# Kernel optimization log

Hardware: AMD Instinct MI355X
Metric: run time of the kernel (lower is better)

The kernel has to match this reference:

```python
import jax, jax.numpy as jnp
import numpy as np

C = 512
NUM_HEADS = 8


def setup_inputs() -> dict:
    key = jax.random.key(0)
    ks = jax.random.split(key, 9)
    s = 1.0 / np.sqrt(C)
    inp = {
        "x": jax.random.normal(ks[0], (2, C, 64, 64), dtype=jnp.float32),
        "Wq": jax.random.uniform(ks[1], (C, C), jnp.float32, -s, s),
        "bq": jax.random.uniform(ks[2], (C,), jnp.float32, -s, s),
        "Wk": jax.random.uniform(ks[3], (C, C), jnp.float32, -s, s),
        "bk": jax.random.uniform(ks[4], (C,), jnp.float32, -s, s),
        "Wv": jax.random.uniform(ks[5], (C, C), jnp.float32, -s, s),
        "bv": jax.random.uniform(ks[6], (C,), jnp.float32, -s, s),
        "Wp": jax.random.uniform(ks[7], (C, C), jnp.float32, -s, s),
        "bp": jax.random.uniform(ks[8], (C,), jnp.float32, -s, s),
    }
    return inp


def _split_heads(t):
    # [B, S, C] -> [B, h, S, d]
    B, S, Ct = t.shape
    return t.reshape(B, S, NUM_HEADS, Ct // NUM_HEADS).transpose(0, 2, 1, 3)


def reference(x, Wq, bq, Wk, bk, Wv, bv, Wp, bp):
    B, Ct, H, W = x.shape
    tok = x.transpose(0, 2, 3, 1).reshape(B, H * W, Ct)  # [B, S, C]
    q = _split_heads(tok @ Wq.T + bq)
    k = _split_heads(tok @ Wk.T + bk)
    v = _split_heads(tok @ Wv.T + bv)
    d = q.shape[-1]
    scores = jnp.einsum("bhsd,bhtd->bhst", q, k) / jnp.sqrt(jnp.float32(d))
    attn = jax.nn.softmax(scores, axis=-1)
    out = jnp.einsum("bhst,bhtd->bhsd", attn, v)
    out = out.transpose(0, 2, 1, 3).reshape(B, H * W, Ct)  # merge heads
    out = out @ Wp.T + bp
    return out.reshape(B, H, W, Ct).transpose(0, 3, 1, 2)
```

## Files before the change

### kernel.cpp

```cpp
#include <hip/hip_runtime.h>
#include <stdint.h>
#include <math.h>

typedef unsigned short u16;
typedef uint32_t u32;
typedef short bf16x8 __attribute__((ext_vector_type(8)));
typedef float f32x4  __attribute__((ext_vector_type(4)));

#define DEV __device__ __forceinline__

DEV u16 f2bf(float f) {
    union { float f; u32 u; } x; x.f = f;
    u32 lsb = (x.u >> 16) & 1u;
    x.u += 0x7fffu + lsb;
    return (u16)(x.u >> 16);
}

DEV u32 pack2(float a, float b) {
    union { float f; u32 u; } x, y; x.f = a; y.f = b;
    return __builtin_amdgcn_perm(y.u + 0x8000u, x.u + 0x8000u, 0x07060302u);
}

#if __has_builtin(__builtin_amdgcn_exp2f)
DEV float fexp2(float x) { return __builtin_amdgcn_exp2f(x); }
#else
DEV float fexp2(float x) { return __expf(x * 0.69314718056f); }
#endif

DEV f32x4 mfma16(bf16x8 a, bf16x8 b, f32x4 c) {
    return __builtin_amdgcn_mfma_f32_16x16x32_bf16(a, b, c, 0, 0, 0);
}

__global__ __launch_bounds__(256) void prep_kernel(const float* __restrict__ x,
                                                   u16* __restrict__ tok,
                                                   const float* __restrict__ w0,
                                                   const float* __restrict__ w1,
                                                   const float* __restrict__ w2,
                                                   const float* __restrict__ w3,
                                                   u16* __restrict__ dst) {
    __shared__ u16 t[64][65];
    const int id = blockIdx.x, tid = threadIdx.x;
    if (id < 1024) {
        const int b = id >> 9, c0 = ((id >> 6) & 7) * 64, s0 = (id & 63) * 64;
        const float* xb = x + ((size_t)b * 512 + c0) * 4096 + s0;
        u16* tb = tok + ((size_t)b * 4096 + s0) * 512 + c0;
        {
            const int jc = tid & 15, i0 = tid >> 4;
#pragma unroll
            for (int ii = 0; ii < 4; ii++) {
                int i = i0 * 4 + ii;
                float4 v = *(const float4*)&xb[(size_t)i * 4096 + jc * 4];
                t[i][jc * 4 + 0] = f2bf(v.x);
                t[i][jc * 4 + 1] = f2bf(v.y);
                t[i][jc * 4 + 2] = f2bf(v.z);
                t[i][jc * 4 + 3] = f2bf(v.w);
            }
        }
        __syncthreads();
        {
            const int j = tid & 31, i0 = tid >> 5;
#pragma unroll
            for (int ii = 0; ii < 8; ii++) {
                int srow = i0 * 8 + ii;
                u32 v = (u32)t[j * 2][srow] | ((u32)t[j * 2 + 1][srow] << 16);
                *(u32*)(&tb[(size_t)srow * 512 + j * 2]) = v;
            }
        }
    } else {
        const int id2 = id - 1024;
        const int j = id2 >> 8;
        const float* src = (j == 0) ? w0 : (j == 1) ? w1 : (j == 2) ? w2 : w3;
        int idx = ((id2 & 255) * 256 + tid) * 4;
        float4 v = *(const float4*)&src[idx];
        uint2 pv;
        pv.x = pack2(v.x, v.y);
        pv.y = pack2(v.z, v.w);
        *(uint2*)&dst[(size_t)j * 262144 + idx] = pv;
    }
}

DEV void proj_core(const u16* __restrict__ W, const float* __restrict__ bias,
                   const u16* __restrict__ Bb, void* __restrict__ out,
                   int b, int mode, float scale,
                   u16 (*__restrict__ Alds)[4096], u16 (*__restrict__ Blds)[4096]) {
    const int tid = threadIdx.x;
    const int wave = tid >> 6, lane = tid & 63, q = lane >> 4, c = lane & 15;
    const int m0 = blockIdx.y * 128, n0 = blockIdx.x * 128;

    const int cs = tid & 15, qs = (tid >> 4) & 3, ms = (tid >> 6) & 3;
    const u16* Asrc0 = W  + (size_t)(m0 + ms * 16 + cs) * 512 + qs * 8;
    const u16* Asrc1 = W  + (size_t)(m0 + (ms + 4) * 16 + cs) * 512 + qs * 8;
    const u16* Bsrc0 = Bb + (size_t)(n0 + ms * 16 + cs) * 512 + qs * 8;
    const u16* Bsrc1 = Bb + (size_t)(n0 + (ms + 4) * 16 + cs) * 512 + qs * 8;

    f32x4 acc[4][4] = {};

    int4 pa0 = *(const int4*)&Asrc0[0];
    int4 pa1 = *(const int4*)&Asrc1[0];
    int4 pb0 = *(const int4*)&Bsrc0[0];
    int4 pb1 = *(const int4*)&Bsrc1[0];
    int4 ha0 = *(const int4*)&Asrc0[32];
    int4 ha1 = *(const int4*)&Asrc1[32];
    int4 hb0 = *(const int4*)&Bsrc0[32];
    int4 hb1 = *(const int4*)&Bsrc1[32];
    *(int4*)&Alds[0][tid * 8]         = pa0;
    *(int4*)&Alds[0][(tid + 256) * 8] = pa1;
    *(int4*)&Blds[0][tid * 8]         = pb0;
    *(int4*)&Blds[0][(tid + 256) * 8] = pb1;
    __syncthreads();

    int p = 0, pw = 1;
    for (int it = 0; it < 16; it++) {
        const int kn = ((it + 2) & 15) * 32;

        int4 na0 = *(const int4*)&Asrc0[kn];
        int4 na1 = *(const int4*)&Asrc1[kn];
        int4 nb0 = *(const int4*)&Bsrc0[kn];
        int4 nb1 = *(const int4*)&Bsrc1[kn];

        bf16x8 af[4], bfr[4];
#pragma unroll
        for (int t = 0; t < 4; t++) {
            int gm = (((wave & 1) * 4 + t) * 4 + q) * 16 + c;
            af[t] = *(const bf16x8*)&Alds[p][gm * 8];
            int gn = (((wave >> 1) * 4 + t) * 4 + q) * 16 + c;
            bfr[t] = *(const bf16x8*)&Blds[p][gn * 8];
        }
#pragma unroll
        for (int mt = 0; mt < 4; mt++)
#pragma unroll
            for (int nt = 0; nt < 4; nt++)
                acc[mt][nt] = mfma16(af[mt], bfr[nt], acc[mt][nt]);

        *(int4*)&Alds[pw][tid * 8]         = ha0;
        *(int4*)&Alds[pw][(tid + 256) * 8] = ha1;
        *(int4*)&Blds[pw][tid * 8]         = hb0;
        *(int4*)&Blds[pw][(tid + 256) * 8] = hb1;
        ha0 = na0; ha1 = na1; hb0 = nb0; hb1 = nb1;
        __syncthreads();
        p = pw; pw = (pw == 2) ? 0 : pw + 1;
    }

    const int mbase = m0 + (wave & 1) * 64, nbase = n0 + (wave >> 1) * 64;
#pragma unroll
    for (int mt = 0; mt < 4; mt++) {
        int co0 = mbase + mt * 16 + q * 4;
        float b0 = bias[co0 + 0], b1 = bias[co0 + 1];
        float b2 = bias[co0 + 2], b3 = bias[co0 + 3];
#pragma unroll
        for (int nt = 0; nt < 4; nt++) {
            int scol = nbase + nt * 16 + c;
            float v0 = (acc[mt][nt][0] + b0) * scale;
            float v1 = (acc[mt][nt][1] + b1) * scale;
            float v2 = (acc[mt][nt][2] + b2) * scale;
            float v3 = (acc[mt][nt][3] + b3) * scale;
            if (mode == 0) {
                uint2 pv; pv.x = pack2(v0, v1); pv.y = pack2(v2, v3);
                size_t idx = ((size_t)(b * 8 + (co0 >> 6)) * 4096 + scol) * 64 + (co0 & 63);
                *(uint2*)&((u16*)out)[idx] = pv;
            } else if (mode == 1) {
                u16* o = (u16*)out;
                o[((size_t)(b * 512 + co0 + 0)) * 4096 + scol] = f2bf(v0);
                o[((size_t)(b * 512 + co0 + 1)) * 4096 + scol] = f2bf(v1);
                o[((size_t)(b * 512 + co0 + 2)) * 4096 + scol] = f2bf(v2);
                o[((size_t)(b * 512 + co0 + 3)) * 4096 + scol] = f2bf(v3);
            } else {
                float* o = (float*)out;
                o[((size_t)(b * 512 + co0 + 0)) * 4096 + scol] = v0;
                o[((size_t)(b * 512 + co0 + 1)) * 4096 + scol] = v1;
                o[((size_t)(b * 512 + co0 + 2)) * 4096 + scol] = v2;
                o[((size_t)(b * 512 + co0 + 3)) * 4096 + scol] = v3;
            }
        }
    }
}

__global__ __launch_bounds__(256) void qkv_kernel(const u16* __restrict__ Wbf,
                                                  const float* __restrict__ bq,
                                                  const float* __restrict__ bk,
                                                  const float* __restrict__ bv,
                                                  const u16* __restrict__ tok,
                                                  u16* __restrict__ Qb,
                                                  u16* __restrict__ Kb,
                                                  u16* __restrict__ Vb) {
    __shared__ u16 Alds[3][4096];
    __shared__ u16 Blds[3][4096];
    const int z = blockIdx.z, j = z >> 1, b = z & 1;
    const u16* W = Wbf + (size_t)j * 262144;
    const float* bias = (j == 0) ? bq : (j == 1) ? bk : bv;
    void* out = (j == 0) ? (void*)Qb : (j == 1) ? (void*)Kb : (void*)Vb;
    const float scale = (j == 0) ? 0.1803368801f : 1.0f;
    const int mode = (j == 2) ? 1 : 0;
    proj_core(W, bias, tok + (size_t)b * (4096 * 512), out, b, mode, scale, Alds, Blds);
}

__global__ __launch_bounds__(256) void projp_kernel(const u16* __restrict__ Wp,
                                                    const float* __restrict__ bp,
                                                    const u16* __restrict__ attout,
                                                    float* __restrict__ out) {
    __shared__ u16 Alds[3][4096];
    __shared__ u16 Blds[3][4096];
    const int b = blockIdx.z;
    proj_core(Wp, bp, attout + (size_t)b * (4096 * 512), out, b, 2, 1.0f, Alds, Blds);
}

__global__ __launch_bounds__(256, 4) void attn_kernel(const u16* __restrict__ Qm,
                                                      const u16* __restrict__ Km,
                                                      const u16* __restrict__ Vm,
                                                      float* __restrict__ Opart,
                                                      float* __restrict__ Lpart) {
    __shared__ u16 Klds[2][4096];
    __shared__ u16 Vlds[2][4096];
    __shared__ u16 Plds[4][1024];
    const int tid = threadIdx.x, wave = tid >> 6, lane = tid & 63;
    const int q = lane >> 4, c = lane & 15;
    const int bhd = blockIdx.y, s0 = blockIdx.x * 128, z = blockIdx.z;
    const int tbase = z * 2048;
    const u16* Qb = Qm + (size_t)bhd * (4096 * 64);
    const u16* Kb = Km + (size_t)bhd * (4096 * 64);
    const u16* Vb = Vm + (size_t)bhd * (64 * 4096);

    bf16x8 qf[2][2];
#pragma unroll
    for (int st = 0; st < 2; st++)
#pragma unroll
        for (int kd = 0; kd < 2; kd++)
            qf[st][kd] = *(const bf16x8*)
                &Qb[(size_t)(s0 + wave * 32 + st * 16 + c) * 64 + kd * 32 + q * 8];

    const int rr = tid & 15, qq = (tid >> 4) & 3, kk = (tid >> 6) & 1;
    const int t40 = tid >> 7, t41 = t40 + 2;
    const u16* Ksrc0 = Kb + (size_t)(tbase + t40 * 16 + rr) * 64 + kk * 32 + qq * 8;
    const u16* Ksrc1 = Kb + (size_t)(tbase + t41 * 16 + rr) * 64 + kk * 32 + qq * 8;
    const u16* Vsrc0 = Vb + (size_t)(t40 * 16 + rr) * 4096 + tbase + kk * 32 + qq * 8;
    const u16* Vsrc1 = Vb + (size_t)(t41 * 16 + rr) * 4096 + tbase + kk * 32 + qq * 8;

    u16* Pwr       = &Plds[wave][(q >> 1) * 128 + (q & 1) * 4 + c * 8];
    const u16* Prd = &Plds[wave][q * 128 + c * 8];

    f32x4 oacc[4][2] = {};
    float lsum[2] = {0.f, 0.f};

    *(int4*)&Klds[0][tid * 8]         = *(const int4*)&Ksrc0[0];
    *(int4*)&Klds[0][(tid + 256) * 8] = *(const int4*)&Ksrc1[0];
    *(int4*)&Vlds[0][tid * 8]         = *(const int4*)&Vsrc0[0];
    *(int4*)&Vlds[0][(tid + 256) * 8] = *(const int4*)&Vsrc1[0];
    __syncthreads();

    for (int it = 0; it < 32; it++) {
        const int p = it & 1;
        const size_t t0n = (size_t)(((it + 1) & 31) * 64);

        int4 kst0 = *(const int4*)&Ksrc0[t0n * 64];
        int4 kst1 = *(const int4*)&Ksrc1[t0n * 64];
        int4 vst0 = *(const int4*)&Vsrc0[t0n];
        int4 vst1 = *(const int4*)&Vsrc1[t0n];

        f32x4 sacc[4][2] = {};
#pragma unroll
        for (int kd = 0; kd < 2; kd++) {
            bf16x8 ka[4];
#pragma unroll
            for (int tt = 0; tt < 4; tt++)
                ka[tt] = *(const bf16x8*)&Klds[p][(((tt * 2 + kd) * 4 + q) * 16 + c) * 8];
#pragma unroll
            for (int tt = 0; tt < 4; tt++)
#pragma unroll
                for (int st = 0; st < 2; st++)
                    sacc[tt][st] = mfma16(ka[tt], qf[st][kd], sacc[tt][st]);
        }

        bf16x8 va[2][4];
#pragma unroll
        for (int kt = 0; kt < 2; kt++)
#pragma unroll
            for (int dt = 0; dt < 4; dt++)
                va[kt][dt] = *(const bf16x8*)&Vlds[p][(((dt * 2 + kt) * 4 + q) * 16 + c) * 8];

#pragma unroll
        for (int st = 0; st < 2; st++) {
#pragma unroll
            for (int tt = 0; tt < 4; tt++) {
                float p0 = fexp2(sacc[tt][st][0]);
                float p1 = fexp2(sacc[tt][st][1]);
                float p2 = fexp2(sacc[tt][st][2]);
                float p3 = fexp2(sacc[tt][st][3]);
                lsum[st] += (p0 + p1) + (p2 + p3);
                uint2 pv; pv.x = pack2(p0, p1); pv.y = pack2(p2, p3);
                *(uint2*)&Pwr[tt * 256] = pv;
            }
#pragma unroll
            for (int kt = 0; kt < 2; kt++) {
                bf16x8 pb = *(const bf16x8*)&Prd[kt * 512];
#pragma unroll
                for (int dt = 0; dt < 4; dt++)
                    oacc[dt][st] = mfma16(va[kt][dt], pb, oacc[dt][st]);
            }
        }

        *(int4*)&Klds[1 - p][tid * 8]         = kst0;
        *(int4*)&Klds[1 - p][(tid + 256) * 8] = kst1;
        *(int4*)&Vlds[1 - p][tid * 8]         = vst0;
        *(int4*)&Vlds[1 - p][(tid + 256) * 8] = vst1;
        __syncthreads();
    }

#pragma unroll
    for (int st = 0; st < 2; st++) {
        float l = lsum[st];
        l += __shfl_xor(l, 16, 64);
        l += __shfl_xor(l, 32, 64);
        const int s = s0 + wave * 32 + st * 16 + c;
        const size_t rowbase = ((size_t)(z * 16 + bhd) * 4096 + s) * 64;
#pragma unroll
        for (int dt = 0; dt < 4; dt++) {
            float4 ov;
            ov.x = oacc[dt][st][0];
            ov.y = oacc[dt][st][1];
            ov.z = oacc[dt][st][2];
            ov.w = oacc[dt][st][3];
            *(float4*)&Opart[rowbase + dt * 16 + q * 4] = ov;
        }
        if (lane < 16)
            Lpart[(size_t)z * 65536 + bhd * 4096 + s0 + wave * 32 + st * 16 + lane] = l;
    }
}

__global__ __launch_bounds__(256) void merge_kernel(const float* __restrict__ Opart,
                                                    const float* __restrict__ Lpart,
                                                    u16* __restrict__ attout) {
    const int i = blockIdx.x * 256 + threadIdx.x;
    const int flat = i * 4;
    const int row = flat >> 6, dv = flat & 63;
    const int bhd = row >> 12, s = row & 4095;
    const float l = Lpart[row] + Lpart[65536 + row];
    const float rl = 1.0f / l;
    const float4 a  = *(const float4*)&Opart[flat];
    const float4 b4 = *(const float4*)&Opart[4194304 + flat];
    uint2 pv;
    pv.x = pack2((a.x + b4.x) * rl, (a.y + b4.y) * rl);
    pv.y = pack2((a.z + b4.z) * rl, (a.w + b4.w) * rl);
    const int b = bhd >> 3, hd = bhd & 7;
    *(uint2*)&attout[((size_t)(b * 4096 + s)) * 512 + hd * 64 + dv] = pv;
}

extern "C" void kernel_launch(void* const* d_in, const int* in_sizes, int n_in,
                              void* d_out, int out_size, void* d_ws, size_t ws_size,
                              hipStream_t stream) {
    (void)in_sizes; (void)n_in; (void)out_size; (void)ws_size;
    const float* x  = (const float*)d_in[0];
    const float* Wq = (const float*)d_in[1];
    const float* bq = (const float*)d_in[2];
    const float* Wk = (const float*)d_in[3];
    const float* bk = (const float*)d_in[4];
    const float* Wv = (const float*)d_in[5];
    const float* bv = (const float*)d_in[6];
    const float* Wp = (const float*)d_in[7];
    const float* bp = (const float*)d_in[8];
    float* out = (float*)d_out;

    const size_t NTOK = (size_t)4 * 1024 * 1024;
    u16* tok = (u16*)d_ws;
    u16* Qb  = tok + NTOK;
    u16* Kb  = Qb + NTOK;
    u16* Vb  = Kb + NTOK;
    u16* Wbf = Vb + NTOK;
    u16* attout = tok;
    float* Opart = (float*)(Wbf + 4 * 262144);
    float* Lpart = Opart + (size_t)2 * 4194304;

    prep_kernel<<<dim3(2048), 256, 0, stream>>>(x, tok, Wq, Wk, Wv, Wp, Wbf);
    qkv_kernel<<<dim3(32, 4, 6), 256, 0, stream>>>(Wbf, bq, bk, bv, tok, Qb, Kb, Vb);
    attn_kernel<<<dim3(32, 16, 2), 256, 0, stream>>>(Qb, Kb, Vb, Opart, Lpart);
    merge_kernel<<<dim3(4096), 256, 0, stream>>>(Opart, Lpart, attout);
    projp_kernel<<<dim3(32, 4, 2), 256, 0, stream>>>(Wbf + 3 * 262144, bp, attout, out);
}
```

Before: 221.0 us.

## Use direct global-to-LDS loads in GEMM and attention; halve projection N-tile

```diff
diff --git a/kernel.cpp b/kernel.cpp
--- a/kernel.cpp
+++ b/kernel.cpp
@@ -8,6 +8,10 @@
 typedef float f32x4  __attribute__((ext_vector_type(4)));
 
 #define DEV __device__ __forceinline__
+
+#define AS1 __attribute__((address_space(1)))
+#define AS3 __attribute__((address_space(3)))
+#define GLOAD16(g, l) __builtin_amdgcn_global_load_lds((const AS1 void*)(g), (AS3 void*)(l), 16, 0, 0)
 
 DEV u16 f2bf(float f) {
     union { float f; u32 u; } x; x.f = f;
@@ -79,13 +83,16 @@
     }
 }
 
+template<int NFR>
 DEV void proj_core(const u16* __restrict__ W, const float* __restrict__ bias,
                    const u16* __restrict__ Bb, void* __restrict__ out,
                    int b, int mode, float scale,
-                   u16 (*__restrict__ Alds)[4096], u16 (*__restrict__ Blds)[4096]) {
+                   u16* __restrict__ Alds, u16* __restrict__ Blds) {
     const int tid = threadIdx.x;
     const int wave = tid >> 6, lane = tid & 63, q = lane >> 4, c = lane & 15;
-    const int m0 = blockIdx.y * 128, n0 = blockIdx.x * 128;
+    const int m0 = blockIdx.y * 128, n0 = blockIdx.x * (NFR * 32);
+    const int BSTR = NFR * 1024;
+    const int wbase = (tid & ~63) * 8;
 
     const int cs = tid & 15, qs = (tid >> 4) & 3, ms = (tid >> 6) & 3;
     const u16* Asrc0 = W  + (size_t)(m0 + ms * 16 + cs) * 512 + qs * 8;
@@ -93,62 +100,55 @@
     const u16* Bsrc0 = Bb + (size_t)(n0 + ms * 16 + cs) * 512 + qs * 8;
     const u16* Bsrc1 = Bb + (size_t)(n0 + (ms + 4) * 16 + cs) * 512 + qs * 8;
 
-    f32x4 acc[4][4] = {};
-
-    int4 pa0 = *(const int4*)&Asrc0[0];
-    int4 pa1 = *(const int4*)&Asrc1[0];
-    int4 pb0 = *(const int4*)&Bsrc0[0];
-    int4 pb1 = *(const int4*)&Bsrc1[0];
-    int4 ha0 = *(const int4*)&Asrc0[32];
-    int4 ha1 = *(const int4*)&Asrc1[32];
-    int4 hb0 = *(const int4*)&Bsrc0[32];
-    int4 hb1 = *(const int4*)&Bsrc1[32];
-    *(int4*)&Alds[0][tid * 8]         = pa0;
-    *(int4*)&Alds[0][(tid + 256) * 8] = pa1;
-    *(int4*)&Blds[0][tid * 8]         = pb0;
-    *(int4*)&Blds[0][(tid + 256) * 8] = pb1;
+    f32x4 acc[4][NFR] = {};
+
+    GLOAD16(Asrc0, Alds + wbase);
+    GLOAD16(Asrc1, Alds + wbase + 2048);
+    GLOAD16(Bsrc0, Blds + wbase);
+    if (NFR == 4) GLOAD16(Bsrc1, Blds + wbase + 2048);
     __syncthreads();
 
-    int p = 0, pw = 1;
     for (int it = 0; it < 16; it++) {
-        const int kn = ((it + 2) & 15) * 32;
-
-        int4 na0 = *(const int4*)&Asrc0[kn];
-        int4 na1 = *(const int4*)&Asrc1[kn];
-        int4 nb0 = *(const int4*)&Bsrc0[kn];
-        int4 nb1 = *(const int4*)&Bsrc1[kn];
-
-        bf16x8 af[4], bfr[4];
+        const int p = it & 1;
+        const int kn = ((it + 1) & 15) * 32;
+
+        u16* Ad = Alds + (1 - p) * 4096 + wbase;
+        u16* Bd = Blds + (1 - p) * BSTR + wbase;
+        GLOAD16(Asrc0 + kn, Ad);
+        GLOAD16(Asrc1 + kn, Ad + 2048);
+        GLOAD16(Bsrc0 + kn, Bd);
+        if (NFR == 4) GLOAD16(Bsrc1 + kn, Bd + 2048);
+
+        const u16* Ap = Alds + p * 4096;
+        const u16* Bp = Blds + p * BSTR;
+        bf16x8 af[4], bfr[NFR];
 #pragma unroll
         for (int t = 0; t < 4; t++) {
             int gm = (((wave & 1) * 4 + t) * 4 + q) * 16 + c;
-            af[t] = *(const bf16x8*)&Alds[p][gm * 8];
-            int gn = (((wave >> 1) * 4 + t) * 4 + q) * 16 + c;
-            bfr[t] = *(const bf16x8*)&Blds[p][gn * 8];
+            af[t] = *(const bf16x8*)&Ap[gm * 8];
+        }
+#pragma unroll
+        for (int t = 0; t < NFR; t++) {
+            int gn = (((wave >> 1) * NFR + t) * 4 + q) * 16 + c;
+            bfr[t] = *(const bf16x8*)&Bp[gn * 8];
         }
 #pragma unroll
         for (int mt = 0; mt < 4; mt++)
 #pragma unroll
-            for (int nt = 0; nt < 4; nt++)
+            for (int nt = 0; nt < NFR; nt++)
                 acc[mt][nt] = mfma16(af[mt], bfr[nt], acc[mt][nt]);
 
-        *(int4*)&Alds[pw][tid * 8]         = ha0;
-        *(int4*)&Alds[pw][(tid + 256) * 8] = ha1;
-        *(int4*)&Blds[pw][tid * 8]         = hb0;
-        *(int4*)&Blds[pw][(tid + 256) * 8] = hb1;
-        ha0 = na0; ha1 = na1; hb0 = nb0; hb1 = nb1;
         __syncthreads();
-        p = pw; pw = (pw == 2) ? 0 : pw + 1;
-    }
-
-    const int mbase = m0 + (wave & 1) * 64, nbase = n0 + (wave >> 1) * 64;
+    }
+
+    const int mbase = m0 + (wave & 1) * 64, nbase = n0 + (wave >> 1) * (NFR * 16);
 #pragma unroll
     for (int mt = 0; mt < 4; mt++) {
         int co0 = mbase + mt * 16 + q * 4;
         float b0 = bias[co0 + 0], b1 = bias[co0 + 1];
         float b2 = bias[co0 + 2], b3 = bias[co0 + 3];
 #pragma unroll
-        for (int nt = 0; nt < 4; nt++) {
+        for (int nt = 0; nt < NFR; nt++) {
             int scol = nbase + nt * 16 + c;
             float v0 = (acc[mt][nt][0] + b0) * scale;
             float v1 = (acc[mt][nt][1] + b1) * scale;
@@ -183,25 +183,25 @@
                                                   u16* __restrict__ Qb,
                                                   u16* __restrict__ Kb,
                                                   u16* __restrict__ Vb) {
-    __shared__ u16 Alds[3][4096];
-    __shared__ u16 Blds[3][4096];
+    __shared__ u16 Alds[2 * 4096];
+    __shared__ u16 Blds[2 * 4096];
     const int z = blockIdx.z, j = z >> 1, b = z & 1;
     const u16* W = Wbf + (size_t)j * 262144;
     const float* bias = (j == 0) ? bq : (j == 1) ? bk : bv;
     void* out = (j == 0) ? (void*)Qb : (j == 1) ? (void*)Kb : (void*)Vb;
     const float scale = (j == 0) ? 0.1803368801f : 1.0f;
     const int mode = (j == 2) ? 1 : 0;
-    proj_core(W, bias, tok + (size_t)b * (4096 * 512), out, b, mode, scale, Alds, Blds);
+    proj_core<4>(W, bias, tok + (size_t)b * (4096 * 512), out, b, mode, scale, Alds, Blds);
 }
 
 __global__ __launch_bounds__(256) void projp_kernel(const u16* __restrict__ Wp,
                                                     const float* __restrict__ bp,
                                                     const u16* __restrict__ attout,
                                                     float* __restrict__ out) {
-    __shared__ u16 Alds[3][4096];
-    __shared__ u16 Blds[3][4096];
+    __shared__ u16 Alds[2 * 4096];
+    __shared__ u16 Blds[2 * 2048];
     const int b = blockIdx.z;
-    proj_core(Wp, bp, attout + (size_t)b * (4096 * 512), out, b, 2, 1.0f, Alds, Blds);
+    proj_core<2>(Wp, bp, attout + (size_t)b * (4096 * 512), out, b, 2, 1.0f, Alds, Blds);
 }
 
 __global__ __launch_bounds__(256, 4) void attn_kernel(const u16* __restrict__ Qm,
@@ -216,6 +216,7 @@
     const int q = lane >> 4, c = lane & 15;
     const int bhd = blockIdx.y, s0 = blockIdx.x * 128, z = blockIdx.z;
     const int tbase = z * 2048;
+    const int wbase = (tid & ~63) * 8;
     const u16* Qb = Qm + (size_t)bhd * (4096 * 64);
     const u16* Kb = Km + (size_t)bhd * (4096 * 64);
     const u16* Vb = Vm + (size_t)bhd * (64 * 4096);
@@ -241,20 +242,20 @@
     f32x4 oacc[4][2] = {};
     float lsum[2] = {0.f, 0.f};
 
-    *(int4*)&Klds[0][tid * 8]         = *(const int4*)&Ksrc0[0];
-    *(int4*)&Klds[0][(tid + 256) * 8] = *(const int4*)&Ksrc1[0];
-    *(int4*)&Vlds[0][tid * 8]         = *(const int4*)&Vsrc0[0];
-    *(int4*)&Vlds[0][(tid + 256) * 8] = *(const int4*)&Vsrc1[0];
+    GLOAD16(Ksrc0, &Klds[0][wbase]);
+    GLOAD16(Ksrc1, &Klds[0][wbase + 2048]);
+    GLOAD16(Vsrc0, &Vlds[0][wbase]);
+    GLOAD16(Vsrc1, &Vlds[0][wbase + 2048]);
     __syncthreads();
 
     for (int it = 0; it < 32; it++) {
         const int p = it & 1;
         const size_t t0n = (size_t)(((it + 1) & 31) * 64);
 
-        int4 kst0 = *(const int4*)&Ksrc0[t0n * 64];
-        int4 kst1 = *(const int4*)&Ksrc1[t0n * 64];
-        int4 vst0 = *(const int4*)&Vsrc0[t0n];
-        int4 vst1 = *(const int4*)&Vsrc1[t0n];
+        GLOAD16(Ksrc0 + t0n * 64, &Klds[1 - p][wbase]);
+        GLOAD16(Ksrc1 + t0n * 64, &Klds[1 - p][wbase + 2048]);
+        GLOAD16(Vsrc0 + t0n,      &Vlds[1 - p][wbase]);
+        GLOAD16(Vsrc1 + t0n,      &Vlds[1 - p][wbase + 2048]);
 
         f32x4 sacc[4][2] = {};
 #pragma unroll
@@ -298,10 +299,6 @@
             }
         }
 
-        *(int4*)&Klds[1 - p][tid * 8]         = kst0;
-        *(int4*)&Klds[1 - p][(tid + 256) * 8] = kst1;
-        *(int4*)&Vlds[1 - p][tid * 8]         = vst0;
-        *(int4*)&Vlds[1 - p][(tid + 256) * 8] = vst1;
         __syncthreads();
     }
 
@@ -373,5 +370,5 @@
     qkv_kernel<<<dim3(32, 4, 6), 256, 0, stream>>>(Wbf, bq, bk, bv, tok, Qb, Kb, Vb);
     attn_kernel<<<dim3(32, 16, 2), 256, 0, stream>>>(Qb, Kb, Vb, Opart, Lpart);
     merge_kernel<<<dim3(4096), 256, 0, stream>>>(Opart, Lpart, attout);
-    projp_kernel<<<dim3(32, 4, 2), 256, 0, stream>>>(Wbf + 3 * 262144, bp, attout, out);
-}
+    projp_kernel<<<dim3(64, 4, 2), 256, 0, stream>>>(Wbf + 3 * 262144, bp, attout, out);
+}
```

After: 232.3 us. 5.1% more time.

## Fuse Q, K, V projections into one kernel sharing token tiles

Applied to the files above, without the earlier changes.

```diff
diff --git a/kernel.cpp b/kernel.cpp
--- a/kernel.cpp
+++ b/kernel.cpp
@@ -79,6 +79,124 @@
     }
 }
 
+__global__ __launch_bounds__(256, 2) void qkv3_kernel(const u16* __restrict__ Wbf,
+                                                      const float* __restrict__ bq,
+                                                      const float* __restrict__ bk,
+                                                      const float* __restrict__ bv,
+                                                      const u16* __restrict__ tok,
+                                                      u16* __restrict__ Qb,
+                                                      u16* __restrict__ Kb,
+                                                      u16* __restrict__ Vb) {
+    __shared__ u16 Alds[3][6144];
+    __shared__ u16 Blds[3][4096];
+    const int tid = threadIdx.x;
+    const int wave = tid >> 6, lane = tid & 63, q = lane >> 4, c = lane & 15;
+    const int n0 = blockIdx.x * 128;
+    const int m0 = blockIdx.y * 64;
+    const int b  = blockIdx.z;
+    const u16* tokb = tok + (size_t)b * (4096 * 512);
+
+    const int cs = tid & 15, qs = (tid >> 4) & 3, ms = tid >> 6;
+    const u16* As0 = Wbf +          (size_t)(m0 + ms * 16 + cs) * 512 + qs * 8;
+    const u16* As1 = Wbf + 262144 + (size_t)(m0 + ms * 16 + cs) * 512 + qs * 8;
+    const u16* As2 = Wbf + 524288 + (size_t)(m0 + ms * 16 + cs) * 512 + qs * 8;
+    const u16* Bsrc0 = tokb + (size_t)(n0 + ms * 16 + cs) * 512 + qs * 8;
+    const u16* Bsrc1 = tokb + (size_t)(n0 + (ms + 4) * 16 + cs) * 512 + qs * 8;
+
+    f32x4 acc[3][2][4] = {};
+
+    int4 pA0 = *(const int4*)&As0[0];
+    int4 pA1 = *(const int4*)&As1[0];
+    int4 pA2 = *(const int4*)&As2[0];
+    int4 pB0 = *(const int4*)&Bsrc0[0];
+    int4 pB1 = *(const int4*)&Bsrc1[0];
+    int4 hA0 = *(const int4*)&As0[32];
+    int4 hA1 = *(const int4*)&As1[32];
+    int4 hA2 = *(const int4*)&As2[32];
+    int4 hB0 = *(const int4*)&Bsrc0[32];
+    int4 hB1 = *(const int4*)&Bsrc1[32];
+    *(int4*)&Alds[0][tid * 8]        = pA0;
+    *(int4*)&Alds[0][2048 + tid * 8] = pA1;
+    *(int4*)&Alds[0][4096 + tid * 8] = pA2;
+    *(int4*)&Blds[0][tid * 8]         = pB0;
+    *(int4*)&Blds[0][(tid + 256) * 8] = pB1;
+    __syncthreads();
+
+    int p = 0, pw = 1;
+    for (int it = 0; it < 16; it++) {
+        const int kn = ((it + 2) & 15) * 32;
+
+        int4 nA0 = *(const int4*)&As0[kn];
+        int4 nA1 = *(const int4*)&As1[kn];
+        int4 nA2 = *(const int4*)&As2[kn];
+        int4 nB0 = *(const int4*)&Bsrc0[kn];
+        int4 nB1 = *(const int4*)&Bsrc1[kn];
+
+        bf16x8 bfr[4];
+#pragma unroll
+        for (int t = 0; t < 4; t++) {
+            int gn = (((wave >> 1) * 4 + t) * 4 + q) * 16 + c;
+            bfr[t] = *(const bf16x8*)&Blds[p][gn * 8];
+        }
+#pragma unroll
+        for (int j = 0; j < 3; j++) {
+            bf16x8 af[2];
+#pragma unroll
+            for (int mt = 0; mt < 2; mt++) {
+                int gm = ((((wave & 1) * 2 + mt) * 4 + q) * 16 + c);
+                af[mt] = *(const bf16x8*)&Alds[p][j * 2048 + gm * 8];
+            }
+#pragma unroll
+            for (int mt = 0; mt < 2; mt++)
+#pragma unroll
+                for (int nt = 0; nt < 4; nt++)
+                    acc[j][mt][nt] = mfma16(af[mt], bfr[nt], acc[j][mt][nt]);
+        }
+
+        *(int4*)&Alds[pw][tid * 8]        = hA0;
+        *(int4*)&Alds[pw][2048 + tid * 8] = hA1;
+        *(int4*)&Alds[pw][4096 + tid * 8] = hA2;
+        *(int4*)&Blds[pw][tid * 8]         = hB0;
+        *(int4*)&Blds[pw][(tid + 256) * 8] = hB1;
+        hA0 = nA0; hA1 = nA1; hA2 = nA2; hB0 = nB0; hB1 = nB1;
+        __syncthreads();
+        p = pw; pw = (pw == 2) ? 0 : pw + 1;
+    }
+
+    const int mbase = m0 + (wave & 1) * 32, nbase = n0 + (wave >> 1) * 64;
+    const int hd = m0 >> 6;
+#pragma unroll
+    for (int j = 0; j < 3; j++) {
+        const float* bias = (j == 0) ? bq : (j == 1) ? bk : bv;
+        const float scale = (j == 0) ? 0.1803368801f : 1.0f;
+        u16* outm = (j == 0) ? Qb : Kb;
+#pragma unroll
+        for (int mt = 0; mt < 2; mt++) {
+            int co0 = mbase + mt * 16 + q * 4;
+            float b0 = bias[co0 + 0], b1 = bias[co0 + 1];
+            float b2 = bias[co0 + 2], b3 = bias[co0 + 3];
+#pragma unroll
+            for (int nt = 0; nt < 4; nt++) {
+                int scol = nbase + nt * 16 + c;
+                float v0 = (acc[j][mt][nt][0] + b0) * scale;
+                float v1 = (acc[j][mt][nt][1] + b1) * scale;
+                float v2 = (acc[j][mt][nt][2] + b2) * scale;
+                float v3 = (acc[j][mt][nt][3] + b3) * scale;
+                if (j < 2) {
+                    uint2 pv; pv.x = pack2(v0, v1); pv.y = pack2(v2, v3);
+                    size_t idx = ((size_t)(b * 8 + hd) * 4096 + scol) * 64 + (co0 & 63);
+                    *(uint2*)&outm[idx] = pv;
+                } else {
+                    Vb[((size_t)(b * 512 + co0 + 0)) * 4096 + scol] = f2bf(v0);
+                    Vb[((size_t)(b * 512 + co0 + 1)) * 4096 + scol] = f2bf(v1);
+                    Vb[((size_t)(b * 512 + co0 + 2)) * 4096 + scol] = f2bf(v2);
+                    Vb[((size_t)(b * 512 + co0 + 3)) * 4096 + scol] = f2bf(v3);
+                }
+            }
+        }
+    }
+}
+
 DEV void proj_core(const u16* __restrict__ W, const float* __restrict__ bias,
                    const u16* __restrict__ Bb, void* __restrict__ out,
                    int b, int mode, float scale,
@@ -154,44 +272,14 @@
             float v1 = (acc[mt][nt][1] + b1) * scale;
             float v2 = (acc[mt][nt][2] + b2) * scale;
             float v3 = (acc[mt][nt][3] + b3) * scale;
-            if (mode == 0) {
-                uint2 pv; pv.x = pack2(v0, v1); pv.y = pack2(v2, v3);
-                size_t idx = ((size_t)(b * 8 + (co0 >> 6)) * 4096 + scol) * 64 + (co0 & 63);
-                *(uint2*)&((u16*)out)[idx] = pv;
-            } else if (mode == 1) {
-                u16* o = (u16*)out;
-                o[((size_t)(b * 512 + co0 + 0)) * 4096 + scol] = f2bf(v0);
-                o[((size_t)(b * 512 + co0 + 1)) * 4096 + scol] = f2bf(v1);
-                o[((size_t)(b * 512 + co0 + 2)) * 4096 + scol] = f2bf(v2);
-                o[((size_t)(b * 512 + co0 + 3)) * 4096 + scol] = f2bf(v3);
-            } else {
-                float* o = (float*)out;
-                o[((size_t)(b * 512 + co0 + 0)) * 4096 + scol] = v0;
-                o[((size_t)(b * 512 + co0 + 1)) * 4096 + scol] = v1;
-                o[((size_t)(b * 512 + co0 + 2)) * 4096 + scol] = v2;
-                o[((size_t)(b * 512 + co0 + 3)) * 4096 + scol] = v3;
-            }
-        }
-    }
-}
-
-__global__ __launch_bounds__(256) void qkv_kernel(const u16* __restrict__ Wbf,
-                                                  const float* __restrict__ bq,
-                                                  const float* __restrict__ bk,
-                                                  const float* __restrict__ bv,
-                                                  const u16* __restrict__ tok,
-                                                  u16* __restrict__ Qb,
-                                                  u16* __restrict__ Kb,
-                                                  u16* __restrict__ Vb) {
-    __shared__ u16 Alds[3][4096];
-    __shared__ u16 Blds[3][4096];
-    const int z = blockIdx.z, j = z >> 1, b = z & 1;
-    const u16* W = Wbf + (size_t)j * 262144;
-    const float* bias = (j == 0) ? bq : (j == 1) ? bk : bv;
-    void* out = (j == 0) ? (void*)Qb : (j == 1) ? (void*)Kb : (void*)Vb;
-    const float scale = (j == 0) ? 0.1803368801f : 1.0f;
-    const int mode = (j == 2) ? 1 : 0;
-    proj_core(W, bias, tok + (size_t)b * (4096 * 512), out, b, mode, scale, Alds, Blds);
+            float* o = (float*)out;
+            o[((size_t)(b * 512 + co0 + 0)) * 4096 + scol] = v0;
+            o[((size_t)(b * 512 + co0 + 1)) * 4096 + scol] = v1;
+            o[((size_t)(b * 512 + co0 + 2)) * 4096 + scol] = v2;
+            o[((size_t)(b * 512 + co0 + 3)) * 4096 + scol] = v3;
+        }
+    }
+    (void)mode;
 }
 
 __global__ __launch_bounds__(256) void projp_kernel(const u16* __restrict__ Wp,
@@ -370,7 +458,7 @@
     float* Lpart = Opart + (size_t)2 * 4194304;
 
     prep_kernel<<<dim3(2048), 256, 0, stream>>>(x, tok, Wq, Wk, Wv, Wp, Wbf);
-    qkv_kernel<<<dim3(32, 4, 6), 256, 0, stream>>>(Wbf, bq, bk, bv, tok, Qb, Kb, Vb);
+    qkv3_kernel<<<dim3(32, 8, 2), 256, 0, stream>>>(Wbf, bq, bk, bv, tok, Qb, Kb, Vb);
     attn_kernel<<<dim3(32, 16, 2), 256, 0, stream>>>(Qb, Kb, Vb, Opart, Lpart);
     merge_kernel<<<dim3(4096), 256, 0, stream>>>(Opart, Lpart, attout);
     projp_kernel<<<dim3(32, 4, 2), 256, 0, stream>>>(Wbf + 3 * 262144, bp, attout, out);
```

Result: no change. 217.9 us (-1.4%).
